# Optimization experiments

Hardware: AMD Instinct MI355X
Metric: run time of the kernel (lower is better)

Reference implementation:

```python
import jax, jax.numpy as jnp
import numpy as np

B, T, K = 256, 512, 128


def setup_inputs() -> dict:
    key = jax.random.key(0)
    k1, k2, k3, k4 = jax.random.split(key, 4)
    emissions = jax.random.normal(k1, (B, T, K), jnp.float32)
    tag_ids = jax.random.randint(k2, (B, T), 0, K, dtype=jnp.int32)
    lengths = jnp.maximum(jax.random.randint(k3, (B,), 0, T + 1, dtype=jnp.int32), 1)
    # learned CRF transition matrix (transition_weight * learning_rate_multiplier)
    transitions = jax.random.normal(k4, (K, K), jnp.float32) * 0.1
    return {"emissions": emissions, "tag_ids": tag_ids, "lengths": lengths,
            "transitions": transitions}


def _log_norm(emissions, transitions, lengths):
    # forward algorithm (log-sum-exp semiring scan over time)
    t = emissions.shape[1]
    alpha0 = emissions[:, 0]  # [B,K]
    valid = jnp.arange(1, t)[:, None] < lengths[None, :]  # [T-1,B]

    def step(alpha, inp):
        emit_t, v = inp  # [B,K], [B]
        new = jax.nn.logsumexp(alpha[:, :, None] + transitions[None], axis=1) + emit_t
        return jnp.where(v[:, None], new, alpha), None

    alpha, _ = jax.lax.scan(step, alpha0, (jnp.swapaxes(emissions[:, 1:], 0, 1), valid))
    return jax.nn.logsumexp(alpha, axis=-1)  # [B]


def _sequence_score(emissions, transitions, tag_ids, lengths):
    t = emissions.shape[1]
    mask = (jnp.arange(t)[None, :] < lengths[:, None]).astype(emissions.dtype)  # [B,T]
    unary = jnp.take_along_axis(emissions, tag_ids[..., None], axis=-1)[..., 0]  # [B,T]
    unary_score = jnp.sum(unary * mask, axis=1)
    pair = transitions[tag_ids[:, :-1], tag_ids[:, 1:]]  # [B,T-1]
    binary_score = jnp.sum(pair * mask[:, 1:], axis=1)  # prefix mask: t+1 valid => t valid
    return unary_score + binary_score


def _viterbi_decode(emissions, transitions, lengths):
    t = emissions.shape[1]
    k = emissions.shape[2]
    v0 = emissions[:, 0]  # [B,K]
    valid = jnp.arange(1, t)[:, None] < lengths[None, :]  # [T-1,B]
    identity_bp = jnp.arange(k, dtype=jnp.int32)[None, :]  # pass-through for padding

    def fwd(v, inp):
        emit_t, va = inp
        scores = v[:, :, None] + transitions[None]  # [B,K,K]
        bp = jnp.argmax(scores, axis=1).astype(jnp.int32)  # [B,K]
        new = jnp.max(scores, axis=1) + emit_t
        v_new = jnp.where(va[:, None], new, v)
        bp = jnp.where(va[:, None], bp, identity_bp)
        return v_new, bp

    v_final, bps = jax.lax.scan(fwd, v0, (jnp.swapaxes(emissions[:, 1:], 0, 1), valid))
    last_tag = jnp.argmax(v_final, axis=-1).astype(jnp.int32)  # [B]

    def back(tag, bp_t):
        prev = jnp.take_along_axis(bp_t, tag[:, None], axis=1)[:, 0]
        return prev, tag  # emit tag_{t+1}, carry tag_t

    first_tag, tags_rest = jax.lax.scan(back, last_tag, bps, reverse=True)
    decoded = jnp.concatenate([first_tag[None], tags_rest], axis=0)  # [T,B]
    return jnp.swapaxes(decoded, 0, 1)  # [B,T]


def reference(emissions, tag_ids, lengths, transitions):
    log_likelihood = _sequence_score(emissions, transitions, tag_ids, lengths) \
        - _log_norm(emissions, transitions, lengths)
    loss = -jnp.mean(log_likelihood)
    decoded = _viterbi_decode(emissions, transitions, lengths)
    mask = (jnp.arange(emissions.shape[1])[None, :] < lengths[:, None]).astype(jnp.int32)
    is_equal = (tag_ids == decoded).astype(jnp.int32)
    tag_accuracy = jnp.sum(is_equal * mask) / jnp.sum(mask)
    return loss, decoded, tag_accuracy
```

## Files before the change

### kernel.cpp

```cpp
#include <hip/hip_runtime.h>

#define T_ 512
#define K_ 128
#define B_ 256

__global__ __launch_bounds__(1024, 4) void crf_main(
    const float* __restrict__ emissions,
    const int* __restrict__ tag_ids,
    const int* __restrict__ lengths,
    const float* __restrict__ transitions,
    float* __restrict__ out,
    float* __restrict__ ws_ll,
    int* __restrict__ ws_cnt)
{
    __shared__ unsigned char bpLDS[T_ * K_];
    __shared__ __align__(16) float eaBuf[2][K_];
    __shared__ __align__(16) float vaBuf[2][K_];
    __shared__ __align__(16) float wmax[2][8];
    __shared__ float redLDS[8];
    __shared__ int   redILDS[8];
    __shared__ unsigned char decLDS[T_];
    __shared__ int ltagLDS;

    const int b   = blockIdx.x;
    const int tid = threadIdx.x;
    const int len = lengths[b];
    const float* emB = emissions + (size_t)b * T_ * K_;
    const int*  tagB = tag_ids + b * T_;

    if (tid < T_) {
        int t = tid;
        float s = 0.f;
        if (t < len) {
            int tg = tagB[t];
            s = emB[t * K_ + tg];
            if (t >= 1) s += transitions[tagB[t - 1] * K_ + tg];
        }
        #pragma unroll
        for (int m = 1; m < 64; m <<= 1) s += __shfl_xor(s, m);
        if ((tid & 63) == 0) redLDS[tid >> 6] = s;
    }

    const int role = tid >> 9;
    const int lin  = tid & 511;
    const int j = lin >> 2;
    const int c = lin & 3;
    const int wv = tid >> 6;

    float tbl[32];
    if (role == 0) {
        #pragma unroll
        for (int k = 0; k < 32; ++k)
            tbl[k] = __expf(transitions[(c * 32 + k) * K_ + j]);
    } else {
        #pragma unroll
        for (int k = 0; k < 32; ++k)
            tbl[k] = transitions[(c * 32 + k) * K_ + j];
    }

    float e0 = emB[j];
    if (role == 0) {
        if (c == 0) eaBuf[0][j] = __expf(e0);
        float wm = e0;
        #pragma unroll
        for (int m = 1; m < 64; m <<= 1) wm = fmaxf(wm, __shfl_xor(wm, m));
        if ((lin & 63) == 0) wmax[0][wv] = wm;
    } else {
        if (c == 0) vaBuf[0][j] = e0;
    }
    __syncthreads();

    int cur = 0;
    float Sprev = 0.f;
    for (int t = 1; t < len; ++t) {
        const float* em = emB + t * K_;
        if (role == 0) {
            float4 w0 = *(const float4*)&wmax[cur][0];
            float4 w1 = *(const float4*)&wmax[cur][4];
            float Scur = fmaxf(fmaxf(fmaxf(w0.x, w0.y), fmaxf(w0.z, w0.w)),
                               fmaxf(fmaxf(w1.x, w1.y), fmaxf(w1.z, w1.w)));
            float emit = em[j];
            const float* ea = &eaBuf[cur][c * 32];
            float a0 = 0.f, a1 = 0.f, a2 = 0.f, a3 = 0.f;
            #pragma unroll
            for (int k = 0; k < 8; ++k) {
                float4 e4 = *(const float4*)(ea + 4 * k);
                a0 = fmaf(e4.x, tbl[4 * k + 0], a0);
                a1 = fmaf(e4.y, tbl[4 * k + 1], a1);
                a2 = fmaf(e4.z, tbl[4 * k + 2], a2);
                a3 = fmaf(e4.w, tbl[4 * k + 3], a3);
            }
            float dot = (a0 + a1) + (a2 + a3);
            dot += __shfl_xor(dot, 1);
            dot += __shfl_xor(dot, 2);
            float anew = __logf(dot) + Sprev + emit;
            if (c == 0) eaBuf[cur ^ 1][j] = __expf(anew - Scur);
            float wm = anew;
            #pragma unroll
            for (int m = 1; m < 64; m <<= 1) wm = fmaxf(wm, __shfl_xor(wm, m));
            if ((lin & 63) == 0) wmax[cur ^ 1][wv] = wm;
            Sprev = Scur;
        } else {
            float emit = em[j];
            const float* va = &vaBuf[cur][c * 32];
            float mB = -3.4028235e38f;
            int arg = 0;
            #pragma unroll
            for (int k = 0; k < 8; ++k) {
                float4 v4 = *(const float4*)(va + 4 * k);
                float s0 = v4.x + tbl[4 * k + 0]; if (s0 > mB) { mB = s0; arg = 4 * k + 0; }
                float s1 = v4.y + tbl[4 * k + 1]; if (s1 > mB) { mB = s1; arg = 4 * k + 1; }
                float s2 = v4.z + tbl[4 * k + 2]; if (s2 > mB) { mB = s2; arg = 4 * k + 2; }
                float s3 = v4.w + tbl[4 * k + 3]; if (s3 > mB) { mB = s3; arg = 4 * k + 3; }
            }
            arg += c * 32;
            #pragma unroll
            for (int d = 1; d < 4; d <<= 1) {
                float om = __shfl_xor(mB, d);
                int   oa = __shfl_xor(arg, d);
                if (om > mB || (om == mB && oa < arg)) { mB = om; arg = oa; }
            }
            if (c == 0) {
                vaBuf[cur ^ 1][j] = mB + emit;
                bpLDS[t * K_ + j] = (unsigned char)arg;
            }
        }
        cur ^= 1;
        __syncthreads();
    }

    float logZv = 0.f;
    if (tid < 64) {
        float s = eaBuf[cur][tid] + eaBuf[cur][tid + 64];
        #pragma unroll
        for (int m = 1; m < 64; m <<= 1) s += __shfl_xor(s, m);
        logZv = Sprev + __logf(s);
    }

    if (tid >= 512 && tid < 576) {
        int l = tid - 512;
        float m = vaBuf[cur][l]; int a = l;
        float v2 = vaBuf[cur][l + 64];
        if (v2 > m) { m = v2; a = l + 64; }
        #pragma unroll
        for (int sft = 1; sft < 64; sft <<= 1) {
            float om = __shfl_xor(m, sft);
            int   oa = __shfl_xor(a, sft);
            if (om > m || (om == m && oa < a)) { m = om; a = oa; }
        }
        if (l == 0) ltagLDS = a;
    }
    __syncthreads();

    if (tid == 0) {
        int tg = ltagLDS;
        for (int t = T_ - 1; t >= 1; --t) {
            decLDS[t] = (unsigned char)tg;
            if (t < len) tg = bpLDS[t * K_ + tg];
        }
        decLDS[0] = (unsigned char)tg;
    }
    __syncthreads();

    if (tid < T_) {
        int t = tid;
        int dv = decLDS[t];
        out[1 + b * T_ + t] = (float)dv;
        int good = (t < len && tagB[t] == dv) ? 1 : 0;
        #pragma unroll
        for (int m = 1; m < 64; m <<= 1) good += __shfl_xor(good, m);
        if ((tid & 63) == 0) redILDS[tid >> 6] = good;
    }
    __syncthreads();

    if (tid == 0) {
        float sc = 0.f; int cnt = 0;
        #pragma unroll
        for (int w = 0; w < 8; ++w) { sc += redLDS[w]; cnt += redILDS[w]; }
        ws_ll[b]  = sc - logZv;
        ws_cnt[b] = cnt;
    }
}

__global__ void crf_final(const float* __restrict__ ws_ll,
                          const int* __restrict__ ws_cnt,
                          const int* __restrict__ lengths,
                          float* __restrict__ out)
{
    __shared__ float sll[4];
    __shared__ int scnt[4], slen[4];
    int tid = threadIdx.x;
    float ll = ws_ll[tid];
    int   cn = ws_cnt[tid];
    int   L  = lengths[tid];
    #pragma unroll
    for (int m = 1; m < 64; m <<= 1) {
        ll += __shfl_xor(ll, m);
        cn += __shfl_xor(cn, m);
        L  += __shfl_xor(L, m);
    }
    if ((tid & 63) == 0) { sll[tid >> 6] = ll; scnt[tid >> 6] = cn; slen[tid >> 6] = L; }
    __syncthreads();
    if (tid == 0) {
        float llS = sll[0] + sll[1] + sll[2] + sll[3];
        int   cS  = scnt[0] + scnt[1] + scnt[2] + scnt[3];
        int   LS  = slen[0] + slen[1] + slen[2] + slen[3];
        out[0] = -llS / (float)B_;
        out[1 + B_ * T_] = (float)cS / (float)LS;
    }
}

extern "C" void kernel_launch(void* const* d_in, const int* in_sizes, int n_in,
                              void* d_out, int out_size, void* d_ws, size_t ws_size,
                              hipStream_t stream) {
    const float* emissions   = (const float*)d_in[0];
    const int*   tag_ids     = (const int*)d_in[1];
    const int*   lengths     = (const int*)d_in[2];
    const float* transitions = (const float*)d_in[3];
    float* out = (float*)d_out;

    float* ws_ll  = (float*)d_ws;
    int*   ws_cnt = (int*)((char*)d_ws + B_ * sizeof(float));

    crf_main<<<B_, 1024, 0, stream>>>(emissions, tag_ids, lengths, transitions,
                                      out, ws_ll, ws_cnt);
    crf_final<<<1, B_, 0, stream>>>(ws_ll, ws_cnt, lengths, out);
}
```

Measured before the change: 662.3 us.

## Use single-element normalizer, prefetch emissions, pin transition table in registers

The per-step max-reduction across waves for the log-sum-exp shift is replaced by taking one element's alpha as the normalizer, which removes a 6-step shuffle reduction and the 8-entry LDS read. The next step's emission is prefetched into a register so the global load is off the critical path. The transition table becomes named scalars with asm fences so it stays in VGPRs instead of possibly spilling from an array. Using an arbitrary element as the shift could risk overflow or underflow if alphas spread widely, though with these transition magnitudes that is probably benign.

```diff
diff --git a/kernel.cpp b/kernel.cpp
--- a/kernel.cpp
+++ b/kernel.cpp
@@ -3,6 +3,8 @@
 #define T_ 512
 #define K_ 128
 #define B_ 256
+
+#define GROUPS(F) F(0) F(1) F(2) F(3) F(4) F(5) F(6) F(7)
 
 __global__ __launch_bounds__(1024, 4) void crf_main(
     const float* __restrict__ emissions,
@@ -16,7 +18,7 @@
     __shared__ unsigned char bpLDS[T_ * K_];
     __shared__ __align__(16) float eaBuf[2][K_];
     __shared__ __align__(16) float vaBuf[2][K_];
-    __shared__ __align__(16) float wmax[2][8];
+    __shared__ float sNorm[2];
     __shared__ float redLDS[8];
     __shared__ int   redILDS[8];
     __shared__ unsigned char decLDS[T_];
@@ -45,74 +47,64 @@
     const int lin  = tid & 511;
     const int j = lin >> 2;
     const int c = lin & 3;
-    const int wv = tid >> 6;
-
-    float tbl[32];
-    if (role == 0) {
-        #pragma unroll
-        for (int k = 0; k < 32; ++k)
-            tbl[k] = __expf(transitions[(c * 32 + k) * K_ + j]);
-    } else {
-        #pragma unroll
-        for (int k = 0; k < 32; ++k)
-            tbl[k] = transitions[(c * 32 + k) * K_ + j];
+
+#define DECLW(g) float w##g##0, w##g##1, w##g##2, w##g##3;
+    GROUPS(DECLW)
+    {
+        const float* wp = transitions + (c * 32) * K_ + j;
+#define LOADW(g) w##g##0 = wp[(4*g+0)*K_]; w##g##1 = wp[(4*g+1)*K_]; \
+                 w##g##2 = wp[(4*g+2)*K_]; w##g##3 = wp[(4*g+3)*K_];
+        GROUPS(LOADW)
+        if (role == 0) {
+#define EXPW(g) w##g##0 = __expf(w##g##0); w##g##1 = __expf(w##g##1); \
+                w##g##2 = __expf(w##g##2); w##g##3 = __expf(w##g##3);
+            GROUPS(EXPW)
+        }
+#define FENCEW(g) asm volatile("" : "+v"(w##g##0), "+v"(w##g##1), "+v"(w##g##2), "+v"(w##g##3));
+        GROUPS(FENCEW)
     }
 
     float e0 = emB[j];
     if (role == 0) {
         if (c == 0) eaBuf[0][j] = __expf(e0);
-        float wm = e0;
-        #pragma unroll
-        for (int m = 1; m < 64; m <<= 1) wm = fmaxf(wm, __shfl_xor(wm, m));
-        if ((lin & 63) == 0) wmax[0][wv] = wm;
+        if (lin == 0) sNorm[0] = e0;
     } else {
         if (c == 0) vaBuf[0][j] = e0;
     }
+    float emNext = emB[K_ + j];
     __syncthreads();
 
     int cur = 0;
     float Sprev = 0.f;
     for (int t = 1; t < len; ++t) {
-        const float* em = emB + t * K_;
+        float emit = emNext;
+        { int tn = (t + 1 < T_) ? (t + 1) : (T_ - 1);
+          emNext = emB[tn * K_ + j]; }
         if (role == 0) {
-            float4 w0 = *(const float4*)&wmax[cur][0];
-            float4 w1 = *(const float4*)&wmax[cur][4];
-            float Scur = fmaxf(fmaxf(fmaxf(w0.x, w0.y), fmaxf(w0.z, w0.w)),
-                               fmaxf(fmaxf(w1.x, w1.y), fmaxf(w1.z, w1.w)));
-            float emit = em[j];
+            float Scur = sNorm[cur];
             const float* ea = &eaBuf[cur][c * 32];
             float a0 = 0.f, a1 = 0.f, a2 = 0.f, a3 = 0.f;
-            #pragma unroll
-            for (int k = 0; k < 8; ++k) {
-                float4 e4 = *(const float4*)(ea + 4 * k);
-                a0 = fmaf(e4.x, tbl[4 * k + 0], a0);
-                a1 = fmaf(e4.y, tbl[4 * k + 1], a1);
-                a2 = fmaf(e4.z, tbl[4 * k + 2], a2);
-                a3 = fmaf(e4.w, tbl[4 * k + 3], a3);
-            }
+#define DOTW(g) { float4 e4 = *(const float4*)(ea + 4*g); \
+                  a0 = fmaf(e4.x, w##g##0, a0); a1 = fmaf(e4.y, w##g##1, a1); \
+                  a2 = fmaf(e4.z, w##g##2, a2); a3 = fmaf(e4.w, w##g##3, a3); }
+            GROUPS(DOTW)
             float dot = (a0 + a1) + (a2 + a3);
             dot += __shfl_xor(dot, 1);
             dot += __shfl_xor(dot, 2);
             float anew = __logf(dot) + Sprev + emit;
             if (c == 0) eaBuf[cur ^ 1][j] = __expf(anew - Scur);
-            float wm = anew;
-            #pragma unroll
-            for (int m = 1; m < 64; m <<= 1) wm = fmaxf(wm, __shfl_xor(wm, m));
-            if ((lin & 63) == 0) wmax[cur ^ 1][wv] = wm;
+            if (lin == 0) sNorm[cur ^ 1] = anew;
             Sprev = Scur;
         } else {
-            float emit = em[j];
             const float* va = &vaBuf[cur][c * 32];
             float mB = -3.4028235e38f;
             int arg = 0;
-            #pragma unroll
-            for (int k = 0; k < 8; ++k) {
-                float4 v4 = *(const float4*)(va + 4 * k);
-                float s0 = v4.x + tbl[4 * k + 0]; if (s0 > mB) { mB = s0; arg = 4 * k + 0; }
-                float s1 = v4.y + tbl[4 * k + 1]; if (s1 > mB) { mB = s1; arg = 4 * k + 1; }
-                float s2 = v4.z + tbl[4 * k + 2]; if (s2 > mB) { mB = s2; arg = 4 * k + 2; }
-                float s3 = v4.w + tbl[4 * k + 3]; if (s3 > mB) { mB = s3; arg = 4 * k + 3; }
-            }
+#define VITW(g) { float4 v4 = *(const float4*)(va + 4*g); \
+        float s0 = v4.x + w##g##0; if (s0 > mB) { mB = s0; arg = 4*g+0; } \
+        float s1 = v4.y + w##g##1; if (s1 > mB) { mB = s1; arg = 4*g+1; } \
+        float s2 = v4.z + w##g##2; if (s2 > mB) { mB = s2; arg = 4*g+2; } \
+        float s3 = v4.w + w##g##3; if (s3 > mB) { mB = s3; arg = 4*g+3; } }
+            GROUPS(VITW)
             arg += c * 32;
             #pragma unroll
             for (int d = 1; d < 4; d <<= 1) {
```

Result: no change. 672.0 us (+1.5%).
